# Kernel optimization log

Hardware: AMD Instinct MI355X
Metric: run time of the kernel (lower is better)

## Reference

```python
import jax, jax.numpy as jnp
import numpy as np

N_SPK = 2048
M_UTT = 8
D_EMB = 512


def setup_inputs() -> dict:
    key = jax.random.key(0)
    k1, = jax.random.split(key, 1)
    embeds = jax.random.normal(k1, (N_SPK * M_UTT, D_EMB), dtype=jnp.float32)
    # module expects L2-normalized utterance embeddings
    embeds = embeds / jnp.linalg.norm(embeds, axis=-1, keepdims=True)
    return {
        "embeds": embeds,
        "w": jnp.asarray(10.0, dtype=jnp.float32),
        "b": jnp.asarray(-5.0, dtype=jnp.float32),
        "n_speakers": N_SPK,
        "m_utterances": M_UTT,
    }


def reference(embeds, w, b, n_speakers, m_utterances):
    N, M = n_speakers, m_utterances
    D = embeds.shape[-1]
    e = embeds.reshape(N, M, D)

    # full centroids (all M utterances), L2-normalized
    centroids = e.mean(axis=1)  # [N, D]
    centroids = centroids / jnp.linalg.norm(centroids, axis=-1, keepdims=True)

    # leave-one-out centroids for same-speaker comparisons
    sums = e.sum(axis=1, keepdims=True)  # [N, 1, D]
    excl = (sums - e) / (M - 1)  # [N, M, D]
    excl = excl / jnp.linalg.norm(excl, axis=-1, keepdims=True)

    # similarity: batched GEMM replaces the original triple loop
    sim = jnp.einsum("nmd,kd->nmk", e, centroids)  # [N, M, N]
    # diagonal (k == i) uses leave-one-out centroid
    diag = jnp.sum(e * excl, axis=-1)  # [N, M]
    idx = jnp.arange(N)
    sim = sim.at[idx, :, idx].set(diag)

    sim = jnp.abs(w) * sim + b

    # cross-entropy with label = own speaker index
    logits = sim.reshape(N * M, N)
    labels = jnp.repeat(jnp.arange(N), M)
    logp = jax.nn.log_softmax(logits, axis=-1)
    loss = -jnp.mean(logp[jnp.arange(N * M), labels])
    return loss
```

## Files before the change

### kernel.cpp

```cpp
#include <hip/hip_runtime.h>
#include <hip/hip_bf16.h>
#include <string.h>

#define N_SPK 2048
#define M_UTT 8
#define D_EMB 512
#define N_ROWS (N_SPK * M_UTT)

using short8 = __attribute__((ext_vector_type(8))) short;
using f32x4  = __attribute__((ext_vector_type(4))) float;

typedef const __attribute__((address_space(1))) unsigned int* gas_p;
typedef __attribute__((address_space(3))) unsigned int* las_p;

__device__ int            g_flag;
__device__ float          g_accum;
__device__ unsigned int   g_done;
__device__ float          g_diag[N_ROWS];
__device__ unsigned short g_cRow[N_SPK * D_EMB];
__device__ float          g_rowsum[N_ROWS * 4];

__device__ __forceinline__ float u2f(unsigned int u) { float f; memcpy(&f, &u, 4); return f; }
__device__ __forceinline__ unsigned int f2u(float f) { unsigned int u; memcpy(&u, &f, 4); return u; }
__device__ __forceinline__ float bflo(unsigned int u) { return u2f(u << 16); }
__device__ __forceinline__ float bfhi(unsigned int u) { return u2f(u & 0xFFFF0000u); }
__device__ __forceinline__ unsigned short f2bf(float f) {
    unsigned int u = f2u(f);
    unsigned int r = u + 0x7FFFu + ((u >> 16) & 1u);
    return (unsigned short)(r >> 16);
}
__device__ __forceinline__ float wsum(float v) {
#pragma unroll
    for (int off = 32; off > 0; off >>= 1) v += __shfl_xor(v, off, 64);
    return v;
}
__device__ __forceinline__ float loadScalar(const void* p, int isbf) {
    float vb = bflo((unsigned int)(*(const unsigned short*)p));
    float vf = *(const float*)p;
    float prim = isbf ? vb : vf;
    float alt  = isbf ? vf : vb;
    float a = fabsf(prim);
    if (isfinite(prim) && a > 1e-6f && a < 1e6f) return prim;
    return alt;
}
__device__ __forceinline__ short8 loadA8(const void* e, long row, int d0, int isbf) {
    if (isbf) {
        return *(const short8*)((const unsigned short*)e + row * D_EMB + d0);
    } else {
        const float* q = (const float*)e + row * D_EMB + d0;
        float4 x = *(const float4*)q;
        float4 y = *(const float4*)(q + 4);
        short8 r;
        r[0] = (short)f2bf(x.x); r[1] = (short)f2bf(x.y);
        r[2] = (short)f2bf(x.z); r[3] = (short)f2bf(x.w);
        r[4] = (short)f2bf(y.x); r[5] = (short)f2bf(y.y);
        r[6] = (short)f2bf(y.z); r[7] = (short)f2bf(y.w);
        return r;
    }
}
__device__ __forceinline__ int detectWave(const void* e, long row, int lane) {
    const unsigned short* q = (const unsigned short*)e + row * D_EMB + lane * 8;
    float p = 0.f;
#pragma unroll
    for (int j = 0; j < 8; ++j) {
        float v = bflo((unsigned int)q[j]);
        p += v * v;
    }
    p = wsum(p);
    return (fabsf(p - 1.0f) < 0.25f) ? 1 : 0;
}

__global__ __launch_bounds__(256) void k1_cent(const void* e) {
    int t = threadIdx.x;
    int wave = t >> 6, lane = t & 63;
    int n = blockIdx.x * 4 + wave;

    int isbf = detectWave(e, (long)n * M_UTT, lane);
    if (blockIdx.x == 0 && t == 0) { g_flag = isbf; g_accum = 0.f; g_done = 0u; }

    float ev[M_UTT][8];
    size_t base = (size_t)n * (M_UTT * D_EMB);
#pragma unroll
    for (int m = 0; m < M_UTT; ++m) {
        size_t idx = base + (size_t)m * D_EMB + (size_t)lane * 8;
        if (isbf) {
            uint4 v = *(const uint4*)((const unsigned short*)e + idx);
            ev[m][0] = bflo(v.x); ev[m][1] = bfhi(v.x);
            ev[m][2] = bflo(v.y); ev[m][3] = bfhi(v.y);
            ev[m][4] = bflo(v.z); ev[m][5] = bfhi(v.z);
            ev[m][6] = bflo(v.w); ev[m][7] = bfhi(v.w);
        } else {
            const float* q = (const float*)e + idx;
            float4 a2 = *(const float4*)q;
            float4 b2 = *(const float4*)(q + 4);
            ev[m][0] = a2.x; ev[m][1] = a2.y; ev[m][2] = a2.z; ev[m][3] = a2.w;
            ev[m][4] = b2.x; ev[m][5] = b2.y; ev[m][6] = b2.z; ev[m][7] = b2.w;
        }
    }

    float s[8];
#pragma unroll
    for (int j = 0; j < 8; ++j) {
        float acc = 0.f;
#pragma unroll
        for (int m = 0; m < M_UTT; ++m) acc += ev[m][j];
        s[j] = acc;
    }

    float p = 0.f;
#pragma unroll
    for (int j = 0; j < 8; ++j) p += s[j] * s[j];
    p = wsum(p);
    float inv = rsqrtf(p);

    unsigned short cw[8];
#pragma unroll
    for (int j = 0; j < 8; ++j) cw[j] = f2bf(s[j] * inv);
    *(short8*)&g_cRow[(size_t)n * D_EMB + lane * 8] = *(short8*)cw;

#pragma unroll
    for (int m = 0; m < M_UTT; ++m) {
        float pd = 0.f, pn = 0.f;
#pragma unroll
        for (int j = 0; j < 8; ++j) {
            float ex = s[j] - ev[m][j];
            pd += ev[m][j] * ex;
            pn += ex * ex;
        }
        pd = wsum(pd);
        pn = wsum(pn);
        if (lane == 0) g_diag[n * M_UTT + m] = pd * rsqrtf(pn);
    }
}

__global__ __launch_bounds__(256, 2) void GE2ELoss_70626442215524_kernel(
        const void* e, const void* wp, const void* bp) {
    __shared__ unsigned short sB[2][2][16 * 512];

    int t = threadIdx.x;
    int wave = t >> 6, lane = t & 63;
    int bx = blockIdx.x;
    int qtr = bx >> 7, rowgrp = bx & 127;
    int rowbase = rowgrp * 128 + wave * 32;
    int isbf = g_flag;
    int quad = lane >> 4, l16 = lane & 15;

    float w_ = fabsf(loadScalar(wp, isbf));
    float b_ = loadScalar(bp, isbf);

    auto stageTile = [&](int buf, int nt2) {
        int c0 = qtr * 512 + nt2 * 32;
#pragma unroll
        for (int g = 0; g < 2; ++g) {
#pragma unroll
            for (int i = 0; i < 4; ++i) {
                int cb = i * 256 + wave * 64;
                int w = cb + lane;
                int col = w & 15;
                int dc = ((w >> 6) << 2) + ((w >> 4) & 3);
                const unsigned short* g_ = &g_cRow[((size_t)(c0 + g * 16 + col) << 9) + dc * 8];
                __builtin_amdgcn_global_load_lds((gas_p)g_, (las_p)&sB[buf][g][cb * 8], 16, 0, 0);
            }
        }
    };

    stageTile(0, 0);

    short8 a[2][16];
#pragma unroll
    for (int s = 0; s < 2; ++s) {
        long row = rowbase + s * 16 + l16;
#pragma unroll
        for (int kt = 0; kt < 16; ++kt)
            a[s][kt] = loadA8(e, row, kt * 32 + quad * 8, isbf);
    }

    float dv[2][4];
    int   dcol[2][4];
#pragma unroll
    for (int s = 0; s < 2; ++s)
#pragma unroll
        for (int r = 0; r < 4; ++r) {
            int grow = rowbase + s * 16 + quad * 4 + r;
            dv[s][r]   = fmaf(w_, g_diag[grow], b_);
            dcol[s][r] = grow >> 3;
        }

    float rsum[2][4];
#pragma unroll
    for (int s = 0; s < 2; ++s)
#pragma unroll
        for (int r = 0; r < 4; ++r) rsum[s][r] = 0.f;

    f32x4 accA[2][2], accB[2][2];

    auto computeTile = [&](f32x4 (&ACC)[2][2], int nt2) {
        int cur = nt2 & 1;
        if (nt2 + 1 < 16) stageTile(cur ^ 1, nt2 + 1);
#pragma unroll
        for (int g = 0; g < 2; ++g) {
            ACC[g][0] = f32x4{0.f, 0.f, 0.f, 0.f};
            ACC[g][1] = f32x4{0.f, 0.f, 0.f, 0.f};
        }
        __builtin_amdgcn_s_setprio(1);
#pragma unroll
        for (int g = 0; g < 2; ++g) {
#pragma unroll
            for (int kt = 0; kt < 16; ++kt) {
                short8 bf = *(const short8*)&sB[cur][g][(kt * 64 + lane) * 8];
                ACC[g][0] = __builtin_amdgcn_mfma_f32_16x16x32_bf16(a[0][kt], bf, ACC[g][0], 0, 0, 0);
                ACC[g][1] = __builtin_amdgcn_mfma_f32_16x16x32_bf16(a[1][kt], bf, ACC[g][1], 0, 0, 0);
            }
        }
        __builtin_amdgcn_s_setprio(0);
    };

    auto epilogTile = [&](f32x4 (&ACC)[2][2], int nt2) {
#pragma unroll
        for (int g = 0; g < 2; ++g) {
            int gcol = qtr * 512 + nt2 * 32 + g * 16 + l16;
#pragma unroll
            for (int s = 0; s < 2; ++s) {
#pragma unroll
                for (int r = 0; r < 4; ++r) {
                    float v = fmaf(w_, ACC[g][s][r], b_);
                    if (gcol == dcol[s][r]) v = dv[s][r];
                    rsum[s][r] += __expf(v);
                }
            }
        }
    };

    __syncthreads();

    computeTile(accA, 0);
    __syncthreads();
    for (int tp = 0; tp < 7; ++tp) {
        computeTile(accB, tp * 2 + 1);
        epilogTile(accA, tp * 2);
        __syncthreads();
        computeTile(accA, tp * 2 + 2);
        epilogTile(accB, tp * 2 + 1);
        __syncthreads();
    }
    computeTile(accB, 15);
    epilogTile(accA, 14);
    epilogTile(accB, 15);

#pragma unroll
    for (int s = 0; s < 2; ++s)
#pragma unroll
        for (int reg = 0; reg < 4; ++reg) {
            float v = rsum[s][reg];
            v += __shfl_xor(v, 1, 64);
            v += __shfl_xor(v, 2, 64);
            v += __shfl_xor(v, 4, 64);
            v += __shfl_xor(v, 8, 64);
            if (l16 == 0) {
                int grow = rowbase + s * 16 + quad * 4 + reg;
                g_rowsum[grow * 4 + qtr] = v;
            }
        }
}

__global__ __launch_bounds__(256) void k3_fin(const void* wp, const void* bp, unsigned int* out) {
    __shared__ float red[4];
    int t = threadIdx.x, bx = blockIdx.x;
    int isbf = g_flag;
    float w_ = fabsf(loadScalar(wp, isbf));
    float b_ = loadScalar(bp, isbf);

    int r = bx * 256 + t;
    float4 q = *(const float4*)&g_rowsum[r * 4];
    float tot = (q.x + q.y) + (q.z + q.w);
    float s = logf(tot) - fmaf(w_, g_diag[r], b_);

    s = wsum(s);
    if ((t & 63) == 0) red[t >> 6] = s;
    __syncthreads();
    if (t == 0) {
        float part = red[0] + red[1] + red[2] + red[3];
        atomicAdd(&g_accum, part);
        __threadfence();
        unsigned int old = atomicAdd(&g_done, 1u);
        if (old == 63u) {
            float loss = atomicAdd(&g_accum, 0.f) * (1.0f / N_ROWS);
            unsigned int h = (unsigned int)f2bf(loss);
            out[0] = (h << 16) | h;
        }
    }
}

extern "C" void kernel_launch(void* const* d_in, const int* in_sizes, int n_in,
                              void* d_out, int out_size, void* d_ws, size_t ws_size,
                              hipStream_t stream) {
    const void* e  = d_in[0];
    const void* wp = d_in[1];
    const void* bp = d_in[2];
    (void)in_sizes; (void)n_in; (void)out_size; (void)d_ws; (void)ws_size;

    k1_cent<<<512, 256, 0, stream>>>(e);
    GE2ELoss_70626442215524_kernel<<<512, 256, 0, stream>>>(e, wp, bp);
    k3_fin<<<64, 256, 0, stream>>>(wp, bp, (unsigned int*)d_out);
}
```

Before: 134.2 us.

## Interleave exp epilogue into MFMA loop and fold finalize into main kernel

The softmax epilogue (scale, diagonal override, exp, accumulate) for the previous tile is now spread across the MFMA k-loop, one element per odd k-step, so the exp work can overlap with matrix instructions instead of running as a separate phase. The separate finalize kernel is removed. The last block to finish the GEMM kernel, found with an atomic counter, now does the log-sum reduction over all rows and writes the loss. This saves one kernel launch but serializes the final reduction onto a single block and adds register pressure in the hot loop.

```diff
diff --git a/kernel.cpp b/kernel.cpp
--- a/kernel.cpp
+++ b/kernel.cpp
@@ -6,6 +6,7 @@
 #define M_UTT 8
 #define D_EMB 512
 #define N_ROWS (N_SPK * M_UTT)
+#define NBLK 512u
 
 using short8 = __attribute__((ext_vector_type(8))) short;
 using f32x4  = __attribute__((ext_vector_type(4))) float;
@@ -14,7 +15,6 @@
 typedef __attribute__((address_space(3))) unsigned int* las_p;
 
 __device__ int            g_flag;
-__device__ float          g_accum;
 __device__ unsigned int   g_done;
 __device__ float          g_diag[N_ROWS];
 __device__ unsigned short g_cRow[N_SPK * D_EMB];
@@ -76,7 +76,7 @@
     int n = blockIdx.x * 4 + wave;
 
     int isbf = detectWave(e, (long)n * M_UTT, lane);
-    if (blockIdx.x == 0 && t == 0) { g_flag = isbf; g_accum = 0.f; g_done = 0u; }
+    if (blockIdx.x == 0 && t == 0) { g_flag = isbf; g_done = 0u; }
 
     float ev[M_UTT][8];
     size_t base = (size_t)n * (M_UTT * D_EMB);
@@ -134,8 +134,10 @@
 }
 
 __global__ __launch_bounds__(256, 2) void GE2ELoss_70626442215524_kernel(
-        const void* e, const void* wp, const void* bp) {
+        const void* e, const void* wp, const void* bp, unsigned int* out) {
     __shared__ unsigned short sB[2][2][16 * 512];
+    __shared__ float red[4];
+    __shared__ unsigned int s_fin;
 
     int t = threadIdx.x;
     int wave = t >> 6, lane = t & 63;
@@ -177,6 +179,7 @@
 
     float dv[2][4];
     int   dcol[2][4];
+    float rsum[2][4];
 #pragma unroll
     for (int s = 0; s < 2; ++s)
 #pragma unroll
@@ -184,19 +187,36 @@
             int grow = rowbase + s * 16 + quad * 4 + r;
             dv[s][r]   = fmaf(w_, g_diag[grow], b_);
             dcol[s][r] = grow >> 3;
-        }
-
-    float rsum[2][4];
-#pragma unroll
-    for (int s = 0; s < 2; ++s)
-#pragma unroll
-        for (int r = 0; r < 4; ++r) rsum[s][r] = 0.f;
+            rsum[s][r] = 0.f;
+        }
 
     f32x4 accA[2][2], accB[2][2];
 
-    auto computeTile = [&](f32x4 (&ACC)[2][2], int nt2) {
+    auto computeTile0 = [&](f32x4 (&ACC)[2][2]) {
+        stageTile(1, 1);
+#pragma unroll
+        for (int g = 0; g < 2; ++g) {
+            ACC[g][0] = f32x4{0.f, 0.f, 0.f, 0.f};
+            ACC[g][1] = f32x4{0.f, 0.f, 0.f, 0.f};
+        }
+        __builtin_amdgcn_s_setprio(1);
+#pragma unroll
+        for (int g = 0; g < 2; ++g) {
+#pragma unroll
+            for (int kt = 0; kt < 16; ++kt) {
+                short8 bf = *(const short8*)&sB[0][g][(kt * 64 + lane) * 8];
+                ACC[g][0] = __builtin_amdgcn_mfma_f32_16x16x32_bf16(a[0][kt], bf, ACC[g][0], 0, 0, 0);
+                ACC[g][1] = __builtin_amdgcn_mfma_f32_16x16x32_bf16(a[1][kt], bf, ACC[g][1], 0, 0, 0);
+            }
+        }
+        __builtin_amdgcn_s_setprio(0);
+    };
+
+    auto computeTileE = [&](f32x4 (&ACC)[2][2], f32x4 (&PRV)[2][2], int nt2) {
         int cur = nt2 & 1;
         if (nt2 + 1 < 16) stageTile(cur ^ 1, nt2 + 1);
+        int pcol0 = qtr * 512 + (nt2 - 1) * 32 + l16;
+        int pcol1 = pcol0 + 16;
 #pragma unroll
         for (int g = 0; g < 2; ++g) {
             ACC[g][0] = f32x4{0.f, 0.f, 0.f, 0.f};
@@ -210,6 +230,16 @@
                 short8 bf = *(const short8*)&sB[cur][g][(kt * 64 + lane) * 8];
                 ACC[g][0] = __builtin_amdgcn_mfma_f32_16x16x32_bf16(a[0][kt], bf, ACC[g][0], 0, 0, 0);
                 ACC[g][1] = __builtin_amdgcn_mfma_f32_16x16x32_bf16(a[1][kt], bf, ACC[g][1], 0, 0, 0);
+                if (kt & 1) {
+                    const int eidx = g * 8 + (kt >> 1);
+                    const int pg = eidx >> 3;
+                    const int s_ = (eidx >> 2) & 1;
+                    const int r_ = eidx & 3;
+                    float v = fmaf(w_, PRV[pg][s_][r_], b_);
+                    int pc = pg ? pcol1 : pcol0;
+                    if (pc == dcol[s_][r_]) v = dv[s_][r_];
+                    rsum[s_][r_] += __expf(v);
+                }
             }
         }
         __builtin_amdgcn_s_setprio(0);
@@ -233,18 +263,15 @@
 
     __syncthreads();
 
-    computeTile(accA, 0);
+    computeTile0(accA);
     __syncthreads();
     for (int tp = 0; tp < 7; ++tp) {
-        computeTile(accB, tp * 2 + 1);
-        epilogTile(accA, tp * 2);
+        computeTileE(accB, accA, tp * 2 + 1);
         __syncthreads();
-        computeTile(accA, tp * 2 + 2);
-        epilogTile(accB, tp * 2 + 1);
+        computeTileE(accA, accB, tp * 2 + 2);
         __syncthreads();
     }
-    computeTile(accB, 15);
-    epilogTile(accA, 14);
+    computeTileE(accB, accA, 15);
     epilogTile(accB, 15);
 
 #pragma unroll
@@ -261,30 +288,30 @@
                 g_rowsum[grow * 4 + qtr] = v;
             }
         }
-}
-
-__global__ __launch_bounds__(256) void k3_fin(const void* wp, const void* bp, unsigned int* out) {
-    __shared__ float red[4];
-    int t = threadIdx.x, bx = blockIdx.x;
-    int isbf = g_flag;
-    float w_ = fabsf(loadScalar(wp, isbf));
-    float b_ = loadScalar(bp, isbf);
-
-    int r = bx * 256 + t;
-    float4 q = *(const float4*)&g_rowsum[r * 4];
-    float tot = (q.x + q.y) + (q.z + q.w);
-    float s = logf(tot) - fmaf(w_, g_diag[r], b_);
-
-    s = wsum(s);
-    if ((t & 63) == 0) red[t >> 6] = s;
+
+    __threadfence();
     __syncthreads();
     if (t == 0) {
-        float part = red[0] + red[1] + red[2] + red[3];
-        atomicAdd(&g_accum, part);
+        unsigned int old = atomicAdd(&g_done, 1u);
+        s_fin = (old == NBLK - 1u) ? 1u : 0u;
+    }
+    __syncthreads();
+
+    if (s_fin) {
         __threadfence();
-        unsigned int old = atomicAdd(&g_done, 1u);
-        if (old == 63u) {
-            float loss = atomicAdd(&g_accum, 0.f) * (1.0f / N_ROWS);
+        float part = 0.f;
+#pragma unroll 4
+        for (int i = 0; i < 64; ++i) {
+            int r = i * 256 + t;
+            float4 q = *(const float4*)&g_rowsum[r * 4];
+            float tot = (q.x + q.y) + (q.z + q.w);
+            part += logf(tot) - fmaf(w_, g_diag[r], b_);
+        }
+        part = wsum(part);
+        if ((t & 63) == 0) red[t >> 6] = part;
+        __syncthreads();
+        if (t == 0) {
+            float loss = (red[0] + red[1] + red[2] + red[3]) * (1.0f / N_ROWS);
             unsigned int h = (unsigned int)f2bf(loss);
             out[0] = (h << 16) | h;
         }
@@ -300,6 +327,6 @@
     (void)in_sizes; (void)n_in; (void)out_size; (void)d_ws; (void)ws_size;
 
     k1_cent<<<512, 256, 0, stream>>>(e);
-    GE2ELoss_70626442215524_kernel<<<512, 256, 0, stream>>>(e, wp, bp);
-    k3_fin<<<64, 256, 0, stream>>>(wp, bp, (unsigned int*)d_out);
-}
+    GE2ELoss_70626442215524_kernel<<<NBLK, 256, 0, stream>>>(
+        e, wp, bp, (unsigned int*)d_out);
+}
```

Measured after the change: 184.0 us. 37.1% more time.
